# Kernel tuning notes

Measured on AMD Instinct MI355X. Metric: run time of the kernel, lower is better.

## Reference

```python
import jax, jax.numpy as jnp
import numpy as np

EMBED_DIM = 64
N_POINTS = 1_000_000


def sinusoidal_embedding(vals, embed_dim):
    # vals: [B] float -> [B, embed_dim]
    half = embed_dim // 2
    log_scale = np.log(10000.0) / (half - 1)
    freqs = jnp.exp(jnp.arange(half, dtype=jnp.float32) * (-log_scale))
    ang = vals[:, None] * freqs[None, :]
    return jnp.concatenate([jnp.sin(ang), jnp.cos(ang)], axis=1)


def embed_mlp(x, w1, b1, w2, b2):
    # Linear -> LeakyReLU(0.1) -> Linear  (embedf / embedm)
    h = jax.nn.leaky_relu(x @ w1.T + b1, negative_slope=0.1)
    return h @ w2.T + b2


def setup_inputs() -> dict:
    key = jax.random.key(0)
    ks = jax.random.split(key, 12)
    d, dh = EMBED_DIM, EMBED_DIM // 2
    s = lambda fan_in: 1.0 / np.sqrt(fan_in)
    return {
        "inputs": jax.random.normal(ks[0], (1, 6, N_POINTS), dtype=jnp.float32),
        "t": jax.random.uniform(ks[1], (1,), dtype=jnp.float32) * 1000.0,
        "mask": jax.random.randint(ks[2], (N_POINTS,), 0, 2, dtype=jnp.int32),
        "pdf": jax.random.normal(ks[3], (N_POINTS, d), dtype=jnp.float32),
        # embedf params: Linear(d,d), Linear(d,d//2)
        "ef_w1": jax.random.uniform(ks[4], (d, d), minval=-s(d), maxval=s(d)),
        "ef_b1": jnp.zeros((d,), jnp.float32),
        "ef_w2": jax.random.uniform(ks[5], (dh, d), minval=-s(d), maxval=s(d)),
        "ef_b2": jnp.zeros((dh,), jnp.float32),
        # embedm params
        "em_w1": jax.random.uniform(ks[6], (d, d), minval=-s(d), maxval=s(d)),
        "em_b1": jnp.zeros((d,), jnp.float32),
        "em_w2": jax.random.uniform(ks[7], (dh, d), minval=-s(d), maxval=s(d)),
        "em_b2": jnp.zeros((dh,), jnp.float32),
    }


def reference(inputs, t, mask, pdf, ef_w1, ef_b1, ef_w2, ef_b2, em_w1, em_b1, em_w2, em_b2):
    n = inputs.shape[-1]
    # pdf branch: [N, 64] -> [1, 64, N]
    pdf_cnl = pdf.T[None]  # [1, 64, N]
    # timestep embedding -> embedf -> broadcast over points
    te = embed_mlp(sinusoidal_embedding(t, EMBED_DIM), ef_w1, ef_b1, ef_w2, ef_b2)  # [1, 32]
    temb = jnp.broadcast_to(te[:, :, None], (te.shape[0], te.shape[1], n))  # [1, 32, N]
    # per-point mask embedding -> embedm
    me = embed_mlp(sinusoidal_embedding(mask.astype(jnp.float32), EMBED_DIM), em_w1, em_b1, em_w2, em_b2)  # [N, 32]
    memb = me.T[None]  # [1, 32, N]
    temb = jnp.concatenate([temb, memb], axis=1)  # [1, 64, N]
    # return conditioning tensors produced by the (truncated) forward prefix
    return jnp.concatenate([pdf_cnl, temb], axis=1)  # [1, 128, N]
```

## Files before the change

### kernel.cpp

```cpp
#include <hip/hip_runtime.h>
#include <math.h>


#define HALF 32
#define PTS 256

typedef float v4f __attribute__((ext_vector_type(4)));

__global__ void embed_small_kernel(const float* __restrict__ t,
                                   const float* __restrict__ ef_w1, const float* __restrict__ ef_b1,
                                   const float* __restrict__ ef_w2, const float* __restrict__ ef_b2,
                                   const float* __restrict__ em_w1, const float* __restrict__ em_b1,
                                   const float* __restrict__ em_w2, const float* __restrict__ em_b2,
                                   float* __restrict__ ws) {
    __shared__ float h[3][64];
    const int tid = threadIdx.x;
    const float log_scale = 0.2970934777f;

    if (tid < 192) {
        const int v = tid >> 6;
        const int j = tid & 63;
        const float val = (v == 0) ? t[0] : (float)(v - 1);
        const float* w1 = (v == 0) ? ef_w1 : em_w1;
        const float* b1 = (v == 0) ? ef_b1 : em_b1;
        float acc = b1[j];
        for (int k = 0; k < HALF; ++k) {
            float f = expf(-(float)k * log_scale);
            float ang = val * f;
            float s, c;
            sincosf(ang, &s, &c);
            acc += s * w1[j * 64 + k] + c * w1[j * 64 + HALF + k];
        }
        h[v][j] = (acc > 0.0f) ? acc : 0.1f * acc;
    }
    __syncthreads();
    if (tid < 96) {
        const int v = tid >> 5;
        const int c = tid & 31;
        const float* w2 = (v == 0) ? ef_w2 : em_w2;
        const float* b2 = (v == 0) ? ef_b2 : em_b2;
        float acc = b2[c];
        for (int j = 0; j < 64; ++j) acc += h[v][j] * w2[c * 64 + j];
        ws[v * 32 + c] = acc;
    }
}

__global__ __launch_bounds__(1024) void pvcnn_cond_kernel(
        const float* __restrict__ pdf,
        const int* __restrict__ mask,
        const float* __restrict__ ws,
        float* __restrict__ out,
        int N) {
    __shared__ float tile[64 * 257];
    __shared__ float emb[96];

    const int tid = threadIdx.x;

    const int nwg = gridDim.x;
    const int q   = nwg >> 3;
    const int r8  = nwg & 7;
    const int xcd = blockIdx.x & 7;
    const int j8  = blockIdx.x >> 3;
    const int bid = (xcd < r8 ? xcd * (q + 1) : r8 * (q + 1) + (xcd - r8) * q) + j8;

    const long long p0 = (long long)bid * PTS;
    const bool full = (p0 + PTS <= (long long)N);

    if (tid < 96) emb[tid] = ws[tid];

    if (full) {
        const v4f* src = (const v4f*)(pdf + p0 * 64);
        #pragma unroll
        for (int it = 0; it < 4; ++it) {
            const int f = tid + it * 1024;
            const int p = f >> 4;
            const int qq = f & 15;
            const v4f v = src[f];
            const int b = (4 * qq) * 257 + p;
            tile[b + 0 * 257] = v.x;
            tile[b + 1 * 257] = v.y;
            tile[b + 2 * 257] = v.z;
            tile[b + 3 * 257] = v.w;
        }
    } else {
        #pragma unroll
        for (int it = 0; it < 4; ++it) {
            const int f = tid + it * 1024;
            const int p = f >> 4;
            const int qq = f & 15;
            v4f v = {0.f, 0.f, 0.f, 0.f};
            if (p0 + p < (long long)N)
                v = ((const v4f*)(pdf + (p0 + p) * 64))[qq];
            const int b = (4 * qq) * 257 + p;
            tile[b + 0 * 257] = v.x;
            tile[b + 1 * 257] = v.y;
            tile[b + 2 * 257] = v.z;
            tile[b + 3 * 257] = v.w;
        }
    }

    const int c  = tid & 255;
    const int rg = tid >> 8;
    const long long col = p0 + c;
    const bool cok = (col < (long long)N);

    int mval = 0;
    if (cok) mval = mask[col];

    __syncthreads();

    if (full) {
        #pragma unroll
        for (int rr = 0; rr < 32; ++rr) {
            const int r = rg + 4 * rr;
            float v;
            if (rr < 16) {
                v = tile[r * 257 + c];
            } else if (rr < 24) {
                v = emb[r - 64];
            } else {
                v = mval ? emb[64 + (r - 96)] : emb[32 + (r - 96)];
            }
            __builtin_nontemporal_store(v, out + (long long)r * N + col);
        }
    } else if (cok) {
        for (int rr = 0; rr < 32; ++rr) {
            const int r = rg + 4 * rr;
            float v;
            if (rr < 16) {
                v = tile[r * 257 + c];
            } else if (rr < 24) {
                v = emb[r - 64];
            } else {
                v = mval ? emb[64 + (r - 96)] : emb[32 + (r - 96)];
            }
            __builtin_nontemporal_store(v, out + (long long)r * N + col);
        }
    }
}

extern "C" void kernel_launch(void* const* d_in, const int* in_sizes, int n_in,
                              void* d_out, int out_size, void* d_ws, size_t ws_size,
                              hipStream_t stream) {
    const float* t     = (const float*)d_in[1];
    const int*   mask  = (const int*)d_in[2];
    const float* pdf   = (const float*)d_in[3];
    const float* ef_w1 = (const float*)d_in[4];
    const float* ef_b1 = (const float*)d_in[5];
    const float* ef_w2 = (const float*)d_in[6];
    const float* ef_b2 = (const float*)d_in[7];
    const float* em_w1 = (const float*)d_in[8];
    const float* em_b1 = (const float*)d_in[9];
    const float* em_w2 = (const float*)d_in[10];
    const float* em_b2 = (const float*)d_in[11];

    float* out = (float*)d_out;
    float* ws  = (float*)d_ws;
    const int N = in_sizes[2];

    embed_small_kernel<<<1, 192, 0, stream>>>(t, ef_w1, ef_b1, ef_w2, ef_b2,
                                              em_w1, em_b1, em_w2, em_b2, ws);

    const int nblocks = (N + PTS - 1) / PTS;
    pvcnn_cond_kernel<<<nblocks, 1024, 0, stream>>>(pdf, mask, ws, out, N);
}
```

Measured before the change: 130.6 us.

## Double points per block, XOR-swizzle LDS tile, read embeddings directly from workspace

```diff
diff --git a/kernel.cpp b/kernel.cpp
--- a/kernel.cpp
+++ b/kernel.cpp
@@ -3,7 +3,7 @@
 
 
 #define HALF 32
-#define PTS 256
+#define PTS 512
 
 typedef float v4f __attribute__((ext_vector_type(4)));
 
@@ -51,8 +51,7 @@
         const float* __restrict__ ws,
         float* __restrict__ out,
         int N) {
-    __shared__ float tile[64 * 257];
-    __shared__ float emb[96];
+    __shared__ float tile[64 * PTS];
 
     const int tid = threadIdx.x;
 
@@ -66,41 +65,39 @@
     const long long p0 = (long long)bid * PTS;
     const bool full = (p0 + PTS <= (long long)N);
 
-    if (tid < 96) emb[tid] = ws[tid];
-
     if (full) {
         const v4f* src = (const v4f*)(pdf + p0 * 64);
         #pragma unroll
-        for (int it = 0; it < 4; ++it) {
+        for (int it = 0; it < 8; ++it) {
             const int f = tid + it * 1024;
             const int p = f >> 4;
-            const int qq = f & 15;
+            const int k = f & 15;
             const v4f v = src[f];
-            const int b = (4 * qq) * 257 + p;
-            tile[b + 0 * 257] = v.x;
-            tile[b + 1 * 257] = v.y;
-            tile[b + 2 * 257] = v.z;
-            tile[b + 3 * 257] = v.w;
+            const int b = (k << 2) * PTS + (p ^ ((k & 7) << 2));
+            tile[b + 0 * PTS] = v.x;
+            tile[b + 1 * PTS] = v.y;
+            tile[b + 2 * PTS] = v.z;
+            tile[b + 3 * PTS] = v.w;
         }
     } else {
         #pragma unroll
-        for (int it = 0; it < 4; ++it) {
+        for (int it = 0; it < 8; ++it) {
             const int f = tid + it * 1024;
             const int p = f >> 4;
-            const int qq = f & 15;
+            const int k = f & 15;
             v4f v = {0.f, 0.f, 0.f, 0.f};
             if (p0 + p < (long long)N)
-                v = ((const v4f*)(pdf + (p0 + p) * 64))[qq];
-            const int b = (4 * qq) * 257 + p;
-            tile[b + 0 * 257] = v.x;
-            tile[b + 1 * 257] = v.y;
-            tile[b + 2 * 257] = v.z;
-            tile[b + 3 * 257] = v.w;
+                v = ((const v4f*)(pdf + (p0 + p) * 64))[k];
+            const int b = (k << 2) * PTS + (p ^ ((k & 7) << 2));
+            tile[b + 0 * PTS] = v.x;
+            tile[b + 1 * PTS] = v.y;
+            tile[b + 2 * PTS] = v.z;
+            tile[b + 3 * PTS] = v.w;
         }
     }
 
-    const int c  = tid & 255;
-    const int rg = tid >> 8;
+    const int c  = tid & 511;
+    const int rg = tid >> 9;
     const long long col = p0 + c;
     const bool cok = (col < (long long)N);
 
@@ -111,28 +108,28 @@
 
     if (full) {
         #pragma unroll
-        for (int rr = 0; rr < 32; ++rr) {
-            const int r = rg + 4 * rr;
+        for (int rr = 0; rr < 64; ++rr) {
+            const int r = rg + 2 * rr;
             float v;
-            if (rr < 16) {
-                v = tile[r * 257 + c];
-            } else if (rr < 24) {
-                v = emb[r - 64];
+            if (rr < 32) {
+                v = tile[r * PTS + (c ^ (((r >> 2) & 7) << 2))];
+            } else if (rr < 48) {
+                v = ws[r - 64];
             } else {
-                v = mval ? emb[64 + (r - 96)] : emb[32 + (r - 96)];
+                v = mval ? ws[64 + (r - 96)] : ws[32 + (r - 96)];
             }
             __builtin_nontemporal_store(v, out + (long long)r * N + col);
         }
     } else if (cok) {
-        for (int rr = 0; rr < 32; ++rr) {
-            const int r = rg + 4 * rr;
+        for (int rr = 0; rr < 64; ++rr) {
+            const int r = rg + 2 * rr;
             float v;
-            if (rr < 16) {
-                v = tile[r * 257 + c];
-            } else if (rr < 24) {
-                v = emb[r - 64];
+            if (rr < 32) {
+                v = tile[r * PTS + (c ^ (((r >> 2) & 7) << 2))];
+            } else if (rr < 48) {
+                v = ws[r - 64];
             } else {
-                v = mval ? emb[64 + (r - 96)] : emb[32 + (r - 96)];
+                v = mval ? ws[64 + (r - 96)] : ws[32 + (r - 96)];
             }
             __builtin_nontemporal_store(v, out + (long long)r * N + col);
         }
```

Result: slower. 141.4 us (+8.3%).
